# Kernel optimization log

Measured on AMD Instinct MI355X. Metric: run time of the kernel, lower is better.

## Reference

```python
import jax, jax.numpy as jnp
import numpy as np

MUL = 16            # multiplicity of 0e and 1o in irreps_in/irreps_out
N_NODES = 12500
N_EDGES = 200000
EDGE_ATTR_DIM = 16
WEIGHT_NUMEL = 4 * MUL * MUL  # 4 uvw paths, mul_sh = 1


def setup_inputs() -> dict:
    key = jax.random.key(0)
    ks = jax.random.split(key, 8)
    node_attr = jax.random.normal(ks[0], (N_NODES, 4 * MUL), dtype=jnp.float32)
    edge_index = jax.random.randint(ks[1], (2, N_EDGES), 0, N_NODES, dtype=jnp.int64)
    edge_attr = jax.random.normal(ks[2], (N_EDGES, EDGE_ATTR_DIM), dtype=jnp.float32)
    edge_sh = jax.random.normal(ks[3], (N_EDGES, 4), dtype=jnp.float32)
    # radial ScalarMLP params: Linear(16,16) + SiLU + Linear(16, weight_numel)
    s1 = 1.0 / np.sqrt(EDGE_ATTR_DIM)
    w1 = jax.random.uniform(ks[4], (EDGE_ATTR_DIM, EDGE_ATTR_DIM), jnp.float32, -s1, s1)
    b1 = jax.random.uniform(ks[5], (EDGE_ATTR_DIM,), jnp.float32, -s1, s1)
    w2 = jax.random.uniform(ks[6], (EDGE_ATTR_DIM, WEIGHT_NUMEL), jnp.float32, -s1, s1)
    b2 = jax.random.uniform(ks[7], (WEIGHT_NUMEL,), jnp.float32, -s1, s1)
    return {"node_attr": node_attr, "edge_index": edge_index, "edge_attr": edge_attr,
            "edge_sh": edge_sh, "w1": w1, "b1": b1, "w2": w2, "b2": b2}


def _conv(node_attr, edge_index, edge_attr, edge_sh, w1, b1, w2, b2):
    N = node_attr.shape[0]
    E = edge_attr.shape[0]
    src, dst = edge_index[0], edge_index[1]

    # gather source node features per edge
    x = node_attr[src]                         # [E, 4*MUL]
    x0 = x[:, :MUL]                            # [E, MUL]    (16x0e)
    x1 = x[:, MUL:].reshape(E, MUL, 3)         # [E, MUL, 3] (16x1o)
    y0 = edge_sh[:, 0]                         # [E]   (1x0e)
    y1 = edge_sh[:, 1:4]                       # [E,3] (1x1o)

    # radial MLP -> per-edge tensor-product weights
    h = jax.nn.silu(edge_attr @ w1 + b1)
    W = (h @ w2 + b2).reshape(E, 4, MUL, MUL)  # 4 uvw paths, [E,4,u,w]

    alpha = 1.0 / np.sqrt(2 * MUL).astype(np.float32)  # path norm: 2 paths * MUL fan-in per out irrep
    inv_sqrt3 = np.float32(1.0 / np.sqrt(3.0))

    # path 0: 0e x 0e -> 0e (CG = 1)
    out0 = jnp.einsum('eu,euw->ew', x0 * y0[:, None], W[:, 0])
    # path 1: 1o x 1o -> 0e (CG = delta_ij / sqrt(3), component-normalized)
    out0 = out0 + inv_sqrt3 * jnp.einsum('eui,ei,euw->ew', x1, y1, W[:, 1])
    # path 2: 0e x 1o -> 1o (CG = identity)
    out1 = jnp.einsum('eu,ei,euw->ewi', x0, y1, W[:, 2])
    # path 3: 1o x 0e -> 1o (CG = identity)
    out1 = out1 + jnp.einsum('eui,e,euw->ewi', x1, y0, W[:, 3])

    out_ij = jnp.concatenate([alpha * out0, (alpha * out1).reshape(E, 3 * MUL)], axis=-1)

    # scatter-mean into destination nodes
    sums = jax.ops.segment_sum(out_ij, dst, num_segments=N)
    counts = jax.ops.segment_sum(jnp.ones((E,), out_ij.dtype), dst, num_segments=N)
    return sums / jnp.maximum(counts, 1.0)[:, None]


def reference(node_attr, edge_index, edge_attr, edge_sh, w1, b1, w2, b2):
    return _conv(node_attr, edge_index, edge_attr, edge_sh, w1, b1, w2, b2)
```

## Files before the change

### kernel.cpp

```cpp
#include <hip/hip_runtime.h>
#include <math.h>

#define E_TOTAL  200000
#define NNODES   12500
#define OUT_ELEM 800000
#define NTILE    (E_TOTAL / 64)

typedef float    f32x4 __attribute__((ext_vector_type(4)));
typedef _Float16 f16x8 __attribute__((ext_vector_type(8)));
typedef _Float16 f16x4 __attribute__((ext_vector_type(4)));
typedef _Float16 f16x2 __attribute__((ext_vector_type(2)));

union AF { f16x8 f; f16x2 h2[4]; };

static const size_t OFF_HEAD   = (size_t)E_TOTAL * 64 * 2;
static const size_t OFF_NEXT   = OFF_HEAD + (size_t)NNODES * 4;
static const size_t OFF_BFRAG  = (OFF_NEXT + (size_t)E_TOTAL * 4 + 15) & ~(size_t)15;
static const size_t WS_NEEDED  = OFF_BFRAG + (size_t)36 * 64 * 8 * 2;

__global__ void k_prep(const float* __restrict__ w2, const float* __restrict__ b2,
                       int* __restrict__ head, _Float16* __restrict__ bfrag) {
    const int g = blockIdx.x * 256 + threadIdx.x;
    if (g < NNODES) head[g] = -1;
    if (g < 36 * 64) {
        const int slot = g >> 6, lane = g & 63;
        const int br = slot / 9, kb = slot - br * 9;
        const int quad = lane >> 4, n = lane & 15;
        const float alpha = 0.17677669529663687f;
        _Float16* dst = bfrag + (size_t)g * 8;
        #pragma unroll
        for (int j = 0; j < 8; ++j) {
            float v;
            if (kb < 8) {
                const int ku = kb * 32 + quad * 8 + j;
                v = w2[(ku >> 4) * 1024 + br * 256 + (ku & 15) * 16 + n];
            } else {
                const int loc = quad * 8 + j;
                v = (loc < 16) ? b2[br * 256 + loc * 16 + n] : 0.0f;
            }
            dst[j] = (_Float16)(alpha * v);
        }
    }
}

__global__ __launch_bounds__(256) void k_conv(
        const float* __restrict__ node_attr,
        const int*   __restrict__ edge_index,
        const float* __restrict__ edge_attr,
        const float* __restrict__ edge_sh,
        const float* __restrict__ w1,
        const float* __restrict__ b1,
        const f16x8* __restrict__ bfrag,
        int* __restrict__ head,
        int* __restrict__ next,
        _Float16* __restrict__ edge_out)
{
    const int t = threadIdx.x;
    __shared__ float  sh_h[64][17];
    __shared__ float4 sh_y[64];
    __shared__ _Float16 sh_s[6][64][24];

    const int ebase = blockIdx.x * 64;
    const float inv_sqrt3 = 0.57735026918962576f;

    if (t < 64) {
        const int e2 = ebase + t;
        const int d = edge_index[E_TOTAL + e2];
        next[e2] = atomicExch(&head[d], e2);
    }

    {
        const int e_loc = t & 63, kq = t >> 6;
        const int e = ebase + e_loc;
        const float* ea = edge_attr + (size_t)e * 16;
        float ear[16];
        #pragma unroll
        for (int dq = 0; dq < 4; ++dq) {
            float4 v = *(const float4*)(ea + dq * 4);
            ear[dq * 4 + 0] = v.x; ear[dq * 4 + 1] = v.y;
            ear[dq * 4 + 2] = v.z; ear[dq * 4 + 3] = v.w;
        }
        float4 acc = *(const float4*)(b1 + kq * 4);
        #pragma unroll
        for (int d = 0; d < 16; ++d) {
            float4 wr = *(const float4*)(w1 + d * 16 + kq * 4);
            acc.x += ear[d] * wr.x; acc.y += ear[d] * wr.y;
            acc.z += ear[d] * wr.z; acc.w += ear[d] * wr.w;
        }
        sh_h[e_loc][kq * 4 + 0] = acc.x / (1.0f + __expf(-acc.x));
        sh_h[e_loc][kq * 4 + 1] = acc.y / (1.0f + __expf(-acc.y));
        sh_h[e_loc][kq * 4 + 2] = acc.z / (1.0f + __expf(-acc.z));
        sh_h[e_loc][kq * 4 + 3] = acc.w / (1.0f + __expf(-acc.w));
    }

    {
        const int e_loc = (t & 15) + ((t >> 6) << 4);
        const int pp = (t >> 4) & 3;
        const int u0 = pp * 4;
        const int e = ebase + e_loc;
        const int src = edge_index[e];
        const float4 yv = *(const float4*)(edge_sh + (size_t)e * 4);
        const float* xp = node_attr + (size_t)src * 64;
        float4 x0v = *(const float4*)(xp + u0);
        float x1v[4][3];
        #pragma unroll
        for (int q = 0; q < 4; ++q)
            #pragma unroll
            for (int i = 0; i < 3; ++i)
                x1v[q][i] = xp[16 + (u0 + q) * 3 + i];
        const float* x0p = &x0v.x;
        f16x4 s0h, s1h, x0h, ah, bh, ch;
        #pragma unroll
        for (int q = 0; q < 4; ++q) {
            s0h[q] = (_Float16)(x0p[q] * yv.x);
            s1h[q] = (_Float16)(inv_sqrt3 * (x1v[q][0] * yv.y + x1v[q][1] * yv.z + x1v[q][2] * yv.w));
            x0h[q] = (_Float16)x0p[q];
            ah[q]  = (_Float16)x1v[q][0];
            bh[q]  = (_Float16)x1v[q][1];
            ch[q]  = (_Float16)x1v[q][2];
        }
        *(f16x4*)&sh_s[0][e_loc][u0] = s0h;
        *(f16x4*)&sh_s[1][e_loc][u0] = s1h;
        *(f16x4*)&sh_s[2][e_loc][u0] = x0h;
        *(f16x4*)&sh_s[3][e_loc][u0] = ah;
        *(f16x4*)&sh_s[4][e_loc][u0] = bh;
        *(f16x4*)&sh_s[5][e_loc][u0] = ch;
        if (pp == 0) sh_y[e_loc] = yv;
    }
    __syncthreads();

    const int lane = t & 63, wv = t >> 6;
    const int m = lane & 15, quad = lane >> 4;
    const int e_loc = wv * 16 + m;
    const int qh = quad >> 1, ql = quad & 1;

    AF svh[6];
    #pragma unroll
    for (int b = 0; b < 6; ++b)
        svh[b].f = *(const f16x8*)&sh_s[b][e_loc][ql * 8];
    float hreg[8];
    #pragma unroll
    for (int kb = 0; kb < 8; ++kb) hreg[kb] = sh_h[e_loc][2 * kb + qh];

    f32x4 acc0  = {0.f, 0.f, 0.f, 0.f};
    f32x4 acc2  = {0.f, 0.f, 0.f, 0.f};
    f32x4 acc3a = {0.f, 0.f, 0.f, 0.f};
    f32x4 acc3b = {0.f, 0.f, 0.f, 0.f};
    f32x4 acc3c = {0.f, 0.f, 0.f, 0.f};

    for (int kb = 0; kb < 9; ++kb) {
        const f16x8 B0 = bfrag[(0 * 9 + kb) * 64 + lane];
        const f16x8 B1 = bfrag[(1 * 9 + kb) * 64 + lane];
        const f16x8 B2 = bfrag[(2 * 9 + kb) * 64 + lane];
        const f16x8 B3 = bfrag[(3 * 9 + kb) * 64 + lane];
        const float selF = (kb < 8) ? hreg[kb] : ((quad < 2) ? 1.0f : 0.0f);
        const _Float16 sh1 = (_Float16)selF;
        const f16x2 sel2 = (f16x2){sh1, sh1};
        AF A[6];
        #pragma unroll
        for (int b = 0; b < 6; ++b)
            #pragma unroll
            for (int p = 0; p < 4; ++p)
                A[b].h2[p] = sel2 * svh[b].h2[p];
        acc0  = __builtin_amdgcn_mfma_f32_16x16x32_f16(A[0].f, B0, acc0, 0, 0, 0);
        acc0  = __builtin_amdgcn_mfma_f32_16x16x32_f16(A[1].f, B1, acc0, 0, 0, 0);
        acc2  = __builtin_amdgcn_mfma_f32_16x16x32_f16(A[2].f, B2, acc2, 0, 0, 0);
        acc3a = __builtin_amdgcn_mfma_f32_16x16x32_f16(A[3].f, B3, acc3a, 0, 0, 0);
        acc3b = __builtin_amdgcn_mfma_f32_16x16x32_f16(A[4].f, B3, acc3b, 0, 0, 0);
        acc3c = __builtin_amdgcn_mfma_f32_16x16x32_f16(A[5].f, B3, acc3c, 0, 0, 0);
    }

    #pragma unroll
    for (int r = 0; r < 4; ++r) {
        const int el = wv * 16 + quad * 4 + r;
        const float4 yv = sh_y[el];
        const float t2v = acc2[r];
        const float o0 = acc0[r];
        const float oa = yv.y * t2v + yv.x * acc3a[r];
        const float ob = yv.z * t2v + yv.x * acc3b[r];
        const float oc = yv.w * t2v + yv.x * acc3c[r];
        f16x4 pk = {(_Float16)o0, (_Float16)oa, (_Float16)ob, (_Float16)oc};
        *(f16x4*)(edge_out + (size_t)(ebase + el) * 64 + m * 4) = pk;
    }
}

__global__ __launch_bounds__(256) void k_gather(const _Float16* __restrict__ edge_out,
                                                const int* __restrict__ head,
                                                const int* __restrict__ next,
                                                float* __restrict__ out) {
    const int t = threadIdx.x;
    const int lane = t & 63;
    const int n = blockIdx.x * 4 + (t >> 6);
    int pe;
    if (lane < 16) pe = lane * 4;
    else { const int idx = lane - 16; const int w = idx / 3; pe = w * 4 + 1 + (idx - w * 3); }
    int j = head[n];
    float acc = 0.0f;
    int deg = 0;
    while (j >= 0) {
        acc += (float)edge_out[(size_t)j * 64 + pe];
        ++deg;
        j = next[j];
    }
    out[n * 64 + lane] = acc / (deg > 0 ? (float)deg : 1.0f);
}

__global__ void k_zero_f(float* __restrict__ out, float* __restrict__ counts) {
    int i = blockIdx.x * 256 + threadIdx.x;
    if (i < OUT_ELEM) out[i] = 0.0f;
    if (i < NNODES)   counts[i] = 0.0f;
}

#define EPB 80
#define NE  8
__global__ __launch_bounds__(256) void k_conv_atomic(
        const float* __restrict__ node_attr,
        const int*   __restrict__ edge_index,
        const float* __restrict__ edge_attr,
        const float* __restrict__ edge_sh,
        const float* __restrict__ w1,
        const float* __restrict__ b1,
        const float* __restrict__ w2,
        const float* __restrict__ b2,
        float* __restrict__ out,
        float* __restrict__ counts)
{
    const int thr   = threadIdx.x;
    const int lane  = thr & 63;
    const int wv    = thr >> 6;
    const int u     = lane >> 2;
    const int wbase = (lane & 3) * 4;

    float4 w2r[16];
    #pragma unroll
    for (int k = 0; k < 16; ++k)
        w2r[k] = *(const float4*)(w2 + k * 1024 + thr * 4);
    const float4 b2r = *(const float4*)(b2 + thr * 4);

    __shared__ __align__(16) float sh_h[NE][16];
    __shared__ float sh_s0[NE][16];
    __shared__ float sh_s1[NE][16];
    __shared__ float sh_x0[NE][16];
    __shared__ float sh_x1[NE][16][3];
    __shared__ float sh_y0[NE];
    __shared__ float sh_y1[NE][3];
    __shared__ int   sh_dst[NE];

    const float alpha     = 0.17677669529663687f;
    const float inv_sqrt3 = 0.57735026918962576f;
    const int e0 = blockIdx.x * EPB;

    for (int batch = 0; batch < EPB / NE; ++batch) {
        const int ebase = e0 + batch * NE;
        if (thr < 128) {
            const int le = thr >> 4, k = thr & 15;
            const int e = ebase + le;
            float acc = b1[k];
            const float* ea = edge_attr + (size_t)e * 16;
            #pragma unroll
            for (int d = 0; d < 16; ++d) acc += ea[d] * w1[d * 16 + k];
            sh_h[le][k] = acc / (1.0f + __expf(-acc));
            if (k == 0) sh_dst[le] = edge_index[E_TOTAL + e];
        } else {
            const int le = (thr - 128) >> 4, uu = thr & 15;
            const int e = ebase + le;
            const int src = edge_index[e];
            const float y0  = edge_sh[e * 4 + 0];
            const float y1a = edge_sh[e * 4 + 1];
            const float y1b = edge_sh[e * 4 + 2];
            const float y1c = edge_sh[e * 4 + 3];
            const float* xp = node_attr + (size_t)src * 64;
            const float x0v = xp[uu];
            const float xa = xp[16 + uu * 3 + 0];
            const float xb = xp[16 + uu * 3 + 1];
            const float xc = xp[16 + uu * 3 + 2];
            sh_x0[le][uu] = x0v;
            sh_x1[le][uu][0] = xa; sh_x1[le][uu][1] = xb; sh_x1[le][uu][2] = xc;
            sh_s0[le][uu] = x0v * y0;
            sh_s1[le][uu] = inv_sqrt3 * (xa * y1a + xb * y1b + xc * y1c);
            if (uu == 0) {
                sh_y0[le] = y0;
                sh_y1[le][0] = y1a; sh_y1[le][1] = y1b; sh_y1[le][2] = y1c;
            }
        }
        __syncthreads();

        for (int le = 0; le < NE; ++le) {
            float W0 = b2r.x, W1 = b2r.y, W2c = b2r.z, W3c = b2r.w;
            const float4* hv = (const float4*)sh_h[le];
            #pragma unroll
            for (int kk = 0; kk < 4; ++kk) {
                const float4 h4 = hv[kk];
                const int kb = kk * 4;
                W0  += h4.x * w2r[kb + 0].x; W1  += h4.x * w2r[kb + 0].y;
                W2c += h4.x * w2r[kb + 0].z; W3c += h4.x * w2r[kb + 0].w;
                W0  += h4.y * w2r[kb + 1].x; W1  += h4.y * w2r[kb + 1].y;
                W2c += h4.y * w2r[kb + 1].z; W3c += h4.y * w2r[kb + 1].w;
                W0  += h4.z * w2r[kb + 2].x; W1  += h4.z * w2r[kb + 2].y;
                W2c += h4.z * w2r[kb + 2].z; W3c += h4.z * w2r[kb + 2].w;
                W0  += h4.w * w2r[kb + 3].x; W1  += h4.w * w2r[kb + 3].y;
                W2c += h4.w * w2r[kb + 3].z; W3c += h4.w * w2r[kb + 3].w;
            }
            const int dst = sh_dst[le];
            float* op = out + (size_t)dst * 64;
            if (wv == 0 || wv == 1) {
                const float s = (wv == 0) ? sh_s0[le][u] : sh_s1[le][u];
                float v0 = s * W0, v1 = s * W1, v2 = s * W2c, v3 = s * W3c;
                #pragma unroll
                for (int off = 4; off <= 32; off <<= 1) {
                    v0 += __shfl_xor(v0, off); v1 += __shfl_xor(v1, off);
                    v2 += __shfl_xor(v2, off); v3 += __shfl_xor(v3, off);
                }
                if (lane < 4) {
                    atomicAdd(op + wbase + 0, alpha * v0);
                    atomicAdd(op + wbase + 1, alpha * v1);
                    atomicAdd(op + wbase + 2, alpha * v2);
                    atomicAdd(op + wbase + 3, alpha * v3);
                    if (wv == 0 && lane == 0) atomicAdd(&counts[dst], 1.0f);
                }
            } else if (wv == 2) {
                const float s = sh_x0[le][u];
                float v0 = s * W0, v1 = s * W1, v2 = s * W2c, v3 = s * W3c;
                #pragma unroll
                for (int off = 4; off <= 32; off <<= 1) {
                    v0 += __shfl_xor(v0, off); v1 += __shfl_xor(v1, off);
                    v2 += __shfl_xor(v2, off); v3 += __shfl_xor(v3, off);
                }
                if (lane < 4) {
                    const float ya = alpha * sh_y1[le][0];
                    const float yb = alpha * sh_y1[le][1];
                    const float yc = alpha * sh_y1[le][2];
                    float vv[4] = {v0, v1, v2, v3};
                    #pragma unroll
                    for (int q = 0; q < 4; ++q) {
                        float* qp = op + 16 + (wbase + q) * 3;
                        atomicAdd(qp + 0, vv[q] * ya);
                        atomicAdd(qp + 1, vv[q] * yb);
                        atomicAdd(qp + 2, vv[q] * yc);
                    }
                }
            } else {
                const float ay0 = alpha * sh_y0[le];
                #pragma unroll
                for (int i = 0; i < 3; ++i) {
                    const float s = sh_x1[le][u][i];
                    float v0 = s * W0, v1 = s * W1, v2 = s * W2c, v3 = s * W3c;
                    #pragma unroll
                    for (int off = 4; off <= 32; off <<= 1) {
                        v0 += __shfl_xor(v0, off); v1 += __shfl_xor(v1, off);
                        v2 += __shfl_xor(v2, off); v3 += __shfl_xor(v3, off);
                    }
                    if (lane < 4) {
                        atomicAdd(op + 16 + (wbase + 0) * 3 + i, ay0 * v0);
                        atomicAdd(op + 16 + (wbase + 1) * 3 + i, ay0 * v1);
                        atomicAdd(op + 16 + (wbase + 2) * 3 + i, ay0 * v2);
                        atomicAdd(op + 16 + (wbase + 3) * 3 + i, ay0 * v3);
                    }
                }
            }
        }
        __syncthreads();
    }
}

__global__ void k_div(float* __restrict__ out, const float* __restrict__ counts) {
    int i = blockIdx.x * 256 + threadIdx.x;
    if (i < OUT_ELEM) {
        float c = counts[i >> 6];
        out[i] *= 1.0f / fmaxf(c, 1.0f);
    }
}

extern "C" void kernel_launch(void* const* d_in, const int* in_sizes, int n_in,
                              void* d_out, int out_size, void* d_ws, size_t ws_size,
                              hipStream_t stream) {
    const float* node_attr  = (const float*)d_in[0];
    const int*   edge_index = (const int*)d_in[1];
    const float* edge_attr  = (const float*)d_in[2];
    const float* edge_sh    = (const float*)d_in[3];
    const float* w1         = (const float*)d_in[4];
    const float* b1         = (const float*)d_in[5];
    const float* w2         = (const float*)d_in[6];
    const float* b2         = (const float*)d_in[7];
    float* out = (float*)d_out;

    if (ws_size >= WS_NEEDED) {
        char* ws = (char*)d_ws;
        _Float16* edge_out = (_Float16*)ws;
        int*      head     = (int*)(ws + OFF_HEAD);
        int*      next     = (int*)(ws + OFF_NEXT);
        _Float16* bfrag    = (_Float16*)(ws + OFF_BFRAG);

        k_prep<<<(NNODES + 255) / 256, 256, 0, stream>>>(w2, b2, head, bfrag);
        k_conv<<<NTILE, 256, 0, stream>>>(
            node_attr, edge_index, edge_attr, edge_sh, w1, b1,
            (const f16x8*)bfrag, head, next, edge_out);
        k_gather<<<NNODES / 4, 256, 0, stream>>>(edge_out, head, next, out);
    } else {
        float* counts = (float*)d_ws;
        k_zero_f<<<(OUT_ELEM + 255) / 256, 256, 0, stream>>>(out, counts);
        k_conv_atomic<<<E_TOTAL / EPB, 256, 0, stream>>>(
            node_attr, edge_index, edge_attr, edge_sh, w1, b1, w2, b2, out, counts);
        k_div<<<(OUT_ELEM + 255) / 256, 256, 0, stream>>>(out, counts);
    }
}
```

Baseline: 130.6 us.

## Replace per-node linked list with fixed-slot padded bucket per destination node

Instead of building a linked list of edges per destination node via atomicExch and walking it serially in the gather kernel, each edge now claims a slot with atomicAdd in a padded per-node bucket of 64 slots and writes its output there directly. The gather kernel then reads a contiguous bucket with independent loads and two accumulators, removing the dependent pointer-chasing latency. In exchange the workspace grows to cover 64 slots per node, and nodes with more than 64 incoming edges would overwrite the last slot and give wrong results, so correctness relies on degrees staying below the cap.

```diff
diff --git a/kernel.cpp b/kernel.cpp
--- a/kernel.cpp
+++ b/kernel.cpp
@@ -5,6 +5,7 @@
 #define NNODES   12500
 #define OUT_ELEM 800000
 #define NTILE    (E_TOTAL / 64)
+#define PAD      64
 
 typedef float    f32x4 __attribute__((ext_vector_type(4)));
 typedef _Float16 f16x8 __attribute__((ext_vector_type(8)));
@@ -13,15 +14,14 @@
 
 union AF { f16x8 f; f16x2 h2[4]; };
 
-static const size_t OFF_HEAD   = (size_t)E_TOTAL * 64 * 2;
-static const size_t OFF_NEXT   = OFF_HEAD + (size_t)NNODES * 4;
-static const size_t OFF_BFRAG  = (OFF_NEXT + (size_t)E_TOTAL * 4 + 15) & ~(size_t)15;
+static const size_t OFF_CNT    = (size_t)NNODES * PAD * 64 * 2;
+static const size_t OFF_BFRAG  = (OFF_CNT + (size_t)NNODES * 4 + 15) & ~(size_t)15;
 static const size_t WS_NEEDED  = OFF_BFRAG + (size_t)36 * 64 * 8 * 2;
 
 __global__ void k_prep(const float* __restrict__ w2, const float* __restrict__ b2,
-                       int* __restrict__ head, _Float16* __restrict__ bfrag) {
+                       int* __restrict__ cnt, _Float16* __restrict__ bfrag) {
     const int g = blockIdx.x * 256 + threadIdx.x;
-    if (g < NNODES) head[g] = -1;
+    if (g < NNODES) cnt[g] = 0;
     if (g < 36 * 64) {
         const int slot = g >> 6, lane = g & 63;
         const int br = slot / 9, kb = slot - br * 9;
@@ -51,14 +51,14 @@
         const float* __restrict__ w1,
         const float* __restrict__ b1,
         const f16x8* __restrict__ bfrag,
-        int* __restrict__ head,
-        int* __restrict__ next,
-        _Float16* __restrict__ edge_out)
+        int* __restrict__ cnt,
+        _Float16* __restrict__ edge_pad)
 {
     const int t = threadIdx.x;
     __shared__ float  sh_h[64][17];
     __shared__ float4 sh_y[64];
     __shared__ _Float16 sh_s[6][64][24];
+    __shared__ int    sh_row[64];
 
     const int ebase = blockIdx.x * 64;
     const float inv_sqrt3 = 0.57735026918962576f;
@@ -66,7 +66,9 @@
     if (t < 64) {
         const int e2 = ebase + t;
         const int d = edge_index[E_TOTAL + e2];
-        next[e2] = atomicExch(&head[d], e2);
+        int slot = atomicAdd(&cnt[d], 1);
+        if (slot >= PAD) slot = PAD - 1;
+        sh_row[t] = d * PAD + slot;
     }
 
     {
@@ -180,13 +182,13 @@
         const float ob = yv.z * t2v + yv.x * acc3b[r];
         const float oc = yv.w * t2v + yv.x * acc3c[r];
         f16x4 pk = {(_Float16)o0, (_Float16)oa, (_Float16)ob, (_Float16)oc};
-        *(f16x4*)(edge_out + (size_t)(ebase + el) * 64 + m * 4) = pk;
-    }
-}
-
-__global__ __launch_bounds__(256) void k_gather(const _Float16* __restrict__ edge_out,
-                                                const int* __restrict__ head,
-                                                const int* __restrict__ next,
+        const int row = sh_row[el];
+        *(f16x4*)(edge_pad + (size_t)row * 64 + m * 4) = pk;
+    }
+}
+
+__global__ __launch_bounds__(256) void k_gather(const _Float16* __restrict__ edge_pad,
+                                                const int* __restrict__ cnt,
                                                 float* __restrict__ out) {
     const int t = threadIdx.x;
     const int lane = t & 63;
@@ -194,15 +196,18 @@
     int pe;
     if (lane < 16) pe = lane * 4;
     else { const int idx = lane - 16; const int w = idx / 3; pe = w * 4 + 1 + (idx - w * 3); }
-    int j = head[n];
-    float acc = 0.0f;
-    int deg = 0;
-    while (j >= 0) {
-        acc += (float)edge_out[(size_t)j * 64 + pe];
-        ++deg;
-        j = next[j];
-    }
-    out[n * 64 + lane] = acc / (deg > 0 ? (float)deg : 1.0f);
+    int c = cnt[n];
+    if (c > PAD) c = PAD;
+    const _Float16* base = edge_pad + (size_t)n * PAD * 64 + pe;
+    float a0 = 0.0f, a1 = 0.0f;
+    int j = 0;
+    for (; j + 2 <= c; j += 2) {
+        a0 += (float)base[(size_t)j * 64];
+        a1 += (float)base[(size_t)(j + 1) * 64];
+    }
+    if (j < c) a0 += (float)base[(size_t)j * 64];
+    const float acc = a0 + a1;
+    out[n * 64 + lane] = acc / (c > 0 ? (float)c : 1.0f);
 }
 
 __global__ void k_zero_f(float* __restrict__ out, float* __restrict__ counts) {
@@ -386,16 +391,15 @@
 
     if (ws_size >= WS_NEEDED) {
         char* ws = (char*)d_ws;
-        _Float16* edge_out = (_Float16*)ws;
-        int*      head     = (int*)(ws + OFF_HEAD);
-        int*      next     = (int*)(ws + OFF_NEXT);
+        _Float16* edge_pad = (_Float16*)ws;
+        int*      cnt      = (int*)(ws + OFF_CNT);
         _Float16* bfrag    = (_Float16*)(ws + OFF_BFRAG);
 
-        k_prep<<<(NNODES + 255) / 256, 256, 0, stream>>>(w2, b2, head, bfrag);
+        k_prep<<<(NNODES + 255) / 256, 256, 0, stream>>>(w2, b2, cnt, bfrag);
         k_conv<<<NTILE, 256, 0, stream>>>(
             node_attr, edge_index, edge_attr, edge_sh, w1, b1,
-            (const f16x8*)bfrag, head, next, edge_out);
-        k_gather<<<NNODES / 4, 256, 0, stream>>>(edge_out, head, next, out);
+            (const f16x8*)bfrag, cnt, edge_pad);
+        k_gather<<<NNODES / 4, 256, 0, stream>>>(edge_pad, cnt, out);
     } else {
         float* counts = (float*)d_ws;
         k_zero_f<<<(OUT_ELEM + 255) / 256, 256, 0, stream>>>(out, counts);
```

After: 137.0 us. 4.9% more time.
